# Optimization experiments

Hardware: AMD Instinct MI355X
Metric: run time of the kernel (lower is better)

The kernel has to match this reference:

```python
import jax, jax.numpy as jnp
import numpy as np

SHAPES = ((100, 100), (50, 50), (25, 25), (13, 13))
LENS = [h * w for h, w in SHAPES]
STARTS = [0]
for n in LENS[:-1]:
    STARTS.append(STARTS[-1] + n)
S_TOT = sum(LENS)  # 13294
B, C, HH, DH, L, P, NQ, NL, FF = 2, 256, 8, 32, 4, 4, 300, 6, 1024
WH = np.array([[w, h] for h, w in SHAPES], np.float32)  # [L,2] (W,H) offset normalizer


def ln(x, g, b):
    m = x.mean(-1, keepdims=True)
    v = ((x - m) ** 2).mean(-1, keepdims=True)
    return (x - m) * jax.lax.rsqrt(v + 1e-5) * g + b


def bilinear(v, grid):
    # v: [N,Hl,Wl,D]; grid: [N,Q,2] in [-1,1]; grid_sample bilinear, align_corners=False, zero padding
    N, Hl, Wl, Dd = v.shape
    x = (grid[..., 0] + 1.0) * 0.5 * Wl - 0.5
    y = (grid[..., 1] + 1.0) * 0.5 * Hl - 0.5
    x0f = jnp.floor(x); y0f = jnp.floor(y)
    wx = x - x0f; wy = y - y0f
    x0 = x0f.astype(jnp.int32); y0 = y0f.astype(jnp.int32)
    vf = v.reshape(N, Hl * Wl, Dd)
    def g(yi, xi):
        valid = (yi >= 0) & (yi < Hl) & (xi >= 0) & (xi < Wl)
        idx = jnp.clip(yi, 0, Hl - 1) * Wl + jnp.clip(xi, 0, Wl - 1)
        return jnp.take_along_axis(vf, idx[..., None], axis=1) * valid[..., None]
    return (((1 - wy) * (1 - wx))[..., None] * g(y0, x0)
            + ((1 - wy) * wx)[..., None] * g(y0, x0 + 1)
            + (wy * (1 - wx))[..., None] * g(y0 + 1, x0)
            + (wy * wx)[..., None] * g(y0 + 1, x0 + 1))


def msda(query, ref, src, so_w, so_b, aw_w, aw_b, vp_w, vp_b, op_w, op_b):
    # query:[B,Lq,C] ref:[B,Lq,L,2] src:[B,S,C]
    Bq, Lq, _ = query.shape
    value = (src @ vp_w.T + vp_b).reshape(Bq, S_TOT, HH, DH)
    offs = (query @ so_w.T + so_b).reshape(Bq, Lq, HH, L, P, 2)
    aw = jax.nn.softmax((query @ aw_w.T + aw_b).reshape(Bq, Lq, HH, L * P), -1)
    aw = aw.reshape(Bq, Lq, HH, L, P)
    loc = ref[:, :, None, :, None, :] + offs / jnp.asarray(WH)[None, None, None, :, None, :]
    grid = 2.0 * loc - 1.0  # [B,Lq,HH,L,P,2]
    out = jnp.zeros((Bq, HH, Lq, DH), query.dtype)
    for l, (Hl, Wl) in enumerate(SHAPES):
        st = STARTS[l]
        v_l = value[:, st:st + Hl * Wl].reshape(Bq, Hl, Wl, HH, DH).transpose(0, 3, 1, 2, 4).reshape(Bq * HH, Hl, Wl, DH)
        g_l = grid[:, :, :, l].transpose(0, 2, 1, 3, 4).reshape(Bq * HH, Lq * P, 2)
        s = bilinear(v_l, g_l).reshape(Bq, HH, Lq, P, DH)
        out = out + jnp.einsum('bqhp,bhqpd->bhqd', aw[:, :, :, l], s)
    out = out.transpose(0, 2, 1, 3).reshape(Bq, Lq, C)
    return out @ op_w.T + op_b


def enc_ref_points():
    refs = []
    for Hl, Wl in SHAPES:
        ry = (jnp.arange(Hl, dtype=jnp.float32) + 0.5) / Hl
        rx = (jnp.arange(Wl, dtype=jnp.float32) + 0.5) / Wl
        gy, gx = jnp.meshgrid(ry, rx, indexing='ij')
        refs.append(jnp.stack([gx.reshape(-1), gy.reshape(-1)], -1))
    r = jnp.concatenate(refs, 0)  # [S,2]; valid_ratios == 1 (no padding)
    return jnp.broadcast_to(r[None, :, None, :], (B, S_TOT, L, 2))


def _forward(src_flatten, pos_flatten, query_embed, level_embed, refp_w, refp_b,
             eso_w, eso_b, eaw_w, eaw_b, evp_w, evp_b, eop_w, eop_b,
             en1_g, en1_b, el1_w, el1_b, el2_w, el2_b, en2_g, en2_b,
             dso_w, dso_b, daw_w, daw_b, dvp_w, dvp_b, dop_w, dop_b,
             dsa_in_w, dsa_in_b, dsa_out_w, dsa_out_b,
             dn1_g, dn1_b, dn2_g, dn2_b, dn3_g, dn3_b,
             dl1_w, dl1_b, dl2_w, dl2_b):
    lev = jnp.concatenate([jnp.broadcast_to(level_embed[l], (LENS[l], C)) for l in range(L)], 0)
    pos = pos_flatten + lev[None]
    memory = src_flatten
    eref = enc_ref_points()
    for i in range(NL):  # encoder
        q = memory + pos
        m2 = msda(q, eref, memory, eso_w[i], eso_b[i], eaw_w[i], eaw_b[i], evp_w[i], evp_b[i], eop_w[i], eop_b[i])
        memory = ln(memory + m2, en1_g[i], en1_b[i])
        f = jax.nn.relu(memory @ el1_w[i].T + el1_b[i]) @ el2_w[i].T + el2_b[i]
        memory = ln(memory + f, en2_g[i], en2_b[i])
    qpos, tgt = jnp.split(query_embed, 2, axis=-1)
    qpos = jnp.broadcast_to(qpos[None], (B, NQ, C))
    tgt = jnp.broadcast_to(tgt[None], (B, NQ, C))
    ref = jax.nn.sigmoid(qpos @ refp_w.T + refp_b)  # [B,NQ,2]
    init_ref = ref
    ref_in = jnp.broadcast_to(ref[:, :, None, :], (B, NQ, L, 2))
    scale = 1.0 / np.sqrt(DH)
    for i in range(NL):  # decoder
        q = tgt + qpos
        wq, wk, wv = jnp.split(dsa_in_w[i], 3, 0)
        bq, bk, bv = jnp.split(dsa_in_b[i], 3, 0)
        qh = (q @ wq.T + bq).reshape(B, NQ, HH, DH).transpose(0, 2, 1, 3)
        kh = (q @ wk.T + bk).reshape(B, NQ, HH, DH).transpose(0, 2, 1, 3)
        vh = (tgt @ wv.T + bv).reshape(B, NQ, HH, DH).transpose(0, 2, 1, 3)
        att = jax.nn.softmax(jnp.einsum('bhqd,bhkd->bhqk', qh, kh) * scale, -1)
        sa = jnp.einsum('bhqk,bhkd->bhqd', att, vh).transpose(0, 2, 1, 3).reshape(B, NQ, C)
        sa = sa @ dsa_out_w[i].T + dsa_out_b[i]
        tgt = ln(tgt + sa, dn2_g[i], dn2_b[i])
        ca = msda(tgt + qpos, ref_in, memory, dso_w[i], dso_b[i], daw_w[i], daw_b[i], dvp_w[i], dvp_b[i], dop_w[i], dop_b[i])
        tgt = ln(tgt + ca, dn1_g[i], dn1_b[i])
        f = jax.nn.relu(tgt @ dl1_w[i].T + dl1_b[i]) @ dl2_w[i].T + dl2_b[i]
        tgt = ln(tgt + f, dn3_g[i], dn3_b[i])
    return tgt, init_ref, ref


def setup_inputs() -> dict:
    ks = iter(jax.random.split(jax.random.key(0), 80))
    def rn(shape, s=0.02):
        return jax.random.normal(next(ks), shape, jnp.float32) * s
    z = lambda shape: jnp.zeros(shape, jnp.float32)
    o = lambda shape: jnp.ones(shape, jnp.float32)
    HLP2, HLP = HH * L * P * 2, HH * L * P
    return {
        'src_flatten': rn((B, S_TOT, C), 1.0),
        'pos_flatten': rn((B, S_TOT, C), 1.0),
        'query_embed': rn((NQ, 2 * C), 1.0),
        'level_embed': rn((L, C), 1.0),
        'refp_w': rn((2, C)), 'refp_b': z((2,)),
        'eso_w': rn((NL, HLP2, C)), 'eso_b': z((NL, HLP2)),
        'eaw_w': rn((NL, HLP, C)), 'eaw_b': z((NL, HLP)),
        'evp_w': rn((NL, C, C)), 'evp_b': z((NL, C)),
        'eop_w': rn((NL, C, C)), 'eop_b': z((NL, C)),
        'en1_g': o((NL, C)), 'en1_b': z((NL, C)),
        'el1_w': rn((NL, FF, C)), 'el1_b': z((NL, FF)),
        'el2_w': rn((NL, C, FF)), 'el2_b': z((NL, C)),
        'en2_g': o((NL, C)), 'en2_b': z((NL, C)),
        'dso_w': rn((NL, HLP2, C)), 'dso_b': z((NL, HLP2)),
        'daw_w': rn((NL, HLP, C)), 'daw_b': z((NL, HLP)),
        'dvp_w': rn((NL, C, C)), 'dvp_b': z((NL, C)),
        'dop_w': rn((NL, C, C)), 'dop_b': z((NL, C)),
        'dsa_in_w': rn((NL, 3 * C, C)), 'dsa_in_b': z((NL, 3 * C)),
        'dsa_out_w': rn((NL, C, C)), 'dsa_out_b': z((NL, C)),
        'dn1_g': o((NL, C)), 'dn1_b': z((NL, C)),
        'dn2_g': o((NL, C)), 'dn2_b': z((NL, C)),
        'dn3_g': o((NL, C)), 'dn3_b': z((NL, C)),
        'dl1_w': rn((NL, FF, C)), 'dl1_b': z((NL, FF)),
        'dl2_w': rn((NL, C, FF)), 'dl2_b': z((NL, C)),
    }


def reference(src_flatten, pos_flatten, query_embed, level_embed, refp_w, refp_b,
              eso_w, eso_b, eaw_w, eaw_b, evp_w, evp_b, eop_w, eop_b,
              en1_g, en1_b, el1_w, el1_b, el2_w, el2_b, en2_g, en2_b,
              dso_w, dso_b, daw_w, daw_b, dvp_w, dvp_b, dop_w, dop_b,
              dsa_in_w, dsa_in_b, dsa_out_w, dsa_out_b,
              dn1_g, dn1_b, dn2_g, dn2_b, dn3_g, dn3_b,
              dl1_w, dl1_b, dl2_w, dl2_b):
    return _forward(src_flatten, pos_flatten, query_embed, level_embed, refp_w, refp_b,
                    eso_w, eso_b, eaw_w, eaw_b, evp_w, evp_b, eop_w, eop_b,
                    en1_g, en1_b, el1_w, el1_b, el2_w, el2_b, en2_g, en2_b,
                    dso_w, dso_b, daw_w, daw_b, dvp_w, dvp_b, dop_w, dop_b,
                    dsa_in_w, dsa_in_b, dsa_out_w, dsa_out_b,
                    dn1_g, dn1_b, dn2_g, dn2_b, dn3_g, dn3_b,
                    dl1_w, dl1_b, dl2_w, dl2_b)
```

## Files before the change

kernel.cpp:

```cpp
#include <hip/hip_runtime.h>

static constexpr int kS  = 13294;
static constexpr int kB  = 2;
static constexpr int kBS = kB * kS;
static constexpr int kC  = 256;
static constexpr int kH  = 8;
static constexpr int kNQ = 300;
static constexpr int kFF = 1024;
static constexpr int kNL = 6;

using short8 = __attribute__((ext_vector_type(8))) short;
using f32x4  = __attribute__((ext_vector_type(4))) float;

__device__ __forceinline__ unsigned short f2b(float f) {
  unsigned u = __builtin_bit_cast(unsigned, f);
  return (unsigned short)((u + 0x7FFF + ((u >> 16) & 1)) >> 16);
}
__device__ __forceinline__ float bf2f(unsigned short u) {
  return __builtin_bit_cast(float, ((unsigned)u) << 16);
}
__device__ __forceinline__ float bflo(unsigned u) {
  return __builtin_bit_cast(float, u << 16);
}
__device__ __forceinline__ float bfhi(unsigned u) {
  return __builtin_bit_cast(float, u & 0xFFFF0000u);
}

#if defined(__has_builtin)
#if __has_builtin(__builtin_amdgcn_global_load_lds)
#define HAS_GLL 1
#endif
#endif
#ifndef HAS_GLL
#define HAS_GLL 0
#endif

#if HAS_GLL
typedef const __attribute__((address_space(1))) void* gas_t;
typedef __attribute__((address_space(3))) void* las_t;
#define GLOAD16(gp, lp) __builtin_amdgcn_global_load_lds((gas_t)(gp), (las_t)(lp), 16, 0, 0)
#endif


template<int ACT, int OBF>
__global__ __launch_bounds__(256) void gemm_mfma(
    const unsigned short* __restrict__ A, const unsigned short* __restrict__ Wt,
    const float* __restrict__ bias, void* __restrict__ outp, int M, int N, int K) {
  __shared__ __align__(16) unsigned short As[128 * 64];
  __shared__ __align__(16) unsigned short Bs[128 * 64];
  const int t = threadIdx.x;
  const int nB = N >> 7;
  const int tot = gridDim.x;
  const int q8 = tot >> 3, r8 = tot & 7;
  const int xcd = blockIdx.x & 7, pos = blockIdx.x >> 3;
  const int wg = (xcd < r8 ? xcd * (q8 + 1) : r8 * (q8 + 1) + (xcd - r8) * q8) + pos;
  const int m0 = (wg / nB) * 128, n0 = (wg % nB) * 128;
  const int wid = t >> 6, lane = t & 63;
  const int wr = wid >> 1, wc = wid & 1;
  const int srow = t >> 3;
  const int scol = (((t & 7) ^ (srow & 7)) * 8);
  const int lr = lane & 15;
  const int q4 = lane >> 4;
  const int e7 = lr & 7;

  f32x4 acc[4][4];
#pragma unroll
  for (int i = 0; i < 4; ++i)
#pragma unroll
    for (int j = 0; j < 4; ++j) acc[i][j] = (f32x4){0.f, 0.f, 0.f, 0.f};

  for (int k0 = 0; k0 < K; k0 += 64) {
#if HAS_GLL
    __syncthreads();
#pragma unroll
    for (int c = 0; c < 4; ++c) {
      int ar = m0 + c * 32 + srow; if (ar >= M) ar = M - 1;
      GLOAD16(A + (size_t)ar * K + k0 + scol, (char*)As + c * 4096 + t * 16);
      int br = n0 + c * 32 + srow; if (br >= N) br = N - 1;
      GLOAD16(Wt + (size_t)br * K + k0 + scol, (char*)Bs + c * 4096 + t * 16);
    }
    __syncthreads();
#else
    short8 ta[4], tb[4];
#pragma unroll
    for (int c = 0; c < 4; ++c) {
      int ar = m0 + c * 32 + srow; if (ar >= M) ar = M - 1;
      ta[c] = *(const short8*)(A + (size_t)ar * K + k0 + scol);
      int br = n0 + c * 32 + srow; if (br >= N) br = N - 1;
      tb[c] = *(const short8*)(Wt + (size_t)br * K + k0 + scol);
    }
    __syncthreads();
#pragma unroll
    for (int c = 0; c < 4; ++c) {
      *(short8*)&As[c * 2048 + t * 8] = ta[c];
      *(short8*)&Bs[c * 2048 + t * 8] = tb[c];
    }
    __syncthreads();
#endif
#pragma unroll
    for (int kk = 0; kk < 2; ++kk) {
      const int pg = (((kk << 2) + q4) ^ e7) * 8;
      short8 af[4], bf[4];
#pragma unroll
      for (int mi = 0; mi < 4; ++mi)
        af[mi] = *(const short8*)&As[(wr * 64 + mi * 16 + lr) * 64 + pg];
#pragma unroll
      for (int ni = 0; ni < 4; ++ni)
        bf[ni] = *(const short8*)&Bs[(wc * 64 + ni * 16 + lr) * 64 + pg];
#pragma unroll
      for (int mi = 0; mi < 4; ++mi)
#pragma unroll
        for (int ni = 0; ni < 4; ++ni)
          acc[mi][ni] = __builtin_amdgcn_mfma_f32_16x16x32_bf16(af[mi], bf[ni], acc[mi][ni], 0, 0, 0);
    }
  }
  const int orow0 = m0 + wr * 64;
  const int ocol = n0 + wc * 64 + lr;
  float bv[4];
#pragma unroll
  for (int ni = 0; ni < 4; ++ni) bv[ni] = bias[ocol + ni * 16];
#pragma unroll
  for (int mi = 0; mi < 4; ++mi) {
#pragma unroll
    for (int j = 0; j < 4; ++j) {
      const int r = orow0 + mi * 16 + q4 * 4 + j;
      if (r < M) {
#pragma unroll
        for (int ni = 0; ni < 4; ++ni) {
          float v = acc[mi][ni][j] + bv[ni];
          if (ACT) v = fmaxf(v, 0.f);
          if (OBF) ((unsigned short*)outp)[(size_t)r * N + ocol + ni * 16] = f2b(v);
          else     ((float*)outp)[(size_t)r * N + ocol + ni * 16] = v;
        }
      }
    }
  }
}

template<int ACT, int OBF>
__global__ __launch_bounds__(256) void gemm_mfma_s(
    const unsigned short* __restrict__ A, const unsigned short* __restrict__ Wt,
    const float* __restrict__ bias, void* __restrict__ outp, int M, int N, int K) {
  __shared__ __align__(16) unsigned short As[64 * 64];
  __shared__ __align__(16) unsigned short Bs[64 * 64];
  const int t = threadIdx.x;
  const int m0 = blockIdx.y * 64, n0 = blockIdx.x * 64;
  const int wid = t >> 6, lane = t & 63;
  const int wr = wid >> 1, wc = wid & 1;
  const int srow = t >> 3;
  const int scol = (((t & 7) ^ (srow & 7)) * 8);
  const int lr = lane & 15;
  const int q4 = lane >> 4;
  const int e7 = lr & 7;

  f32x4 acc[2][2];
#pragma unroll
  for (int i = 0; i < 2; ++i)
#pragma unroll
    for (int j = 0; j < 2; ++j) acc[i][j] = (f32x4){0.f, 0.f, 0.f, 0.f};

  for (int k0 = 0; k0 < K; k0 += 64) {
#if HAS_GLL
    __syncthreads();
#pragma unroll
    for (int c = 0; c < 2; ++c) {
      int ar = m0 + c * 32 + srow; if (ar >= M) ar = M - 1;
      GLOAD16(A + (size_t)ar * K + k0 + scol, (char*)As + c * 4096 + t * 16);
      int br = n0 + c * 32 + srow; if (br >= N) br = N - 1;
      GLOAD16(Wt + (size_t)br * K + k0 + scol, (char*)Bs + c * 4096 + t * 16);
    }
    __syncthreads();
#else
    short8 ta[2], tb[2];
#pragma unroll
    for (int c = 0; c < 2; ++c) {
      int ar = m0 + c * 32 + srow; if (ar >= M) ar = M - 1;
      ta[c] = *(const short8*)(A + (size_t)ar * K + k0 + scol);
      int br = n0 + c * 32 + srow; if (br >= N) br = N - 1;
      tb[c] = *(const short8*)(Wt + (size_t)br * K + k0 + scol);
    }
    __syncthreads();
#pragma unroll
    for (int c = 0; c < 2; ++c) {
      *(short8*)&As[c * 2048 + t * 8] = ta[c];
      *(short8*)&Bs[c * 2048 + t * 8] = tb[c];
    }
    __syncthreads();
#endif
#pragma unroll
    for (int kk = 0; kk < 2; ++kk) {
      const int pg = (((kk << 2) + q4) ^ e7) * 8;
      short8 af[2], bf[2];
#pragma unroll
      for (int mi = 0; mi < 2; ++mi)
        af[mi] = *(const short8*)&As[(wr * 32 + mi * 16 + lr) * 64 + pg];
#pragma unroll
      for (int ni = 0; ni < 2; ++ni)
        bf[ni] = *(const short8*)&Bs[(wc * 32 + ni * 16 + lr) * 64 + pg];
#pragma unroll
      for (int mi = 0; mi < 2; ++mi)
#pragma unroll
        for (int ni = 0; ni < 2; ++ni)
          acc[mi][ni] = __builtin_amdgcn_mfma_f32_16x16x32_bf16(af[mi], bf[ni], acc[mi][ni], 0, 0, 0);
    }
  }
  const int orow0 = m0 + wr * 32;
  const int ocol = n0 + wc * 32 + lr;
  float bv[2];
#pragma unroll
  for (int ni = 0; ni < 2; ++ni) bv[ni] = bias[ocol + ni * 16];
#pragma unroll
  for (int mi = 0; mi < 2; ++mi) {
#pragma unroll
    for (int j = 0; j < 4; ++j) {
      const int r = orow0 + mi * 16 + q4 * 4 + j;
      if (r < M) {
#pragma unroll
        for (int ni = 0; ni < 2; ++ni) {
          float v = acc[mi][ni][j] + bv[ni];
          if (ACT) v = fmaxf(v, 0.f);
          if (OBF) ((unsigned short*)outp)[(size_t)r * N + ocol + ni * 16] = f2b(v);
          else     ((float*)outp)[(size_t)r * N + ocol + ni * 16] = v;
        }
      }
    }
  }
}

template<int WRITEQ, int WRITEF>
__global__ __launch_bounds__(256) void gemm_ln_k(
    const unsigned short* __restrict__ A, const unsigned short* __restrict__ Wt,
    const float* __restrict__ bias, const unsigned short* __restrict__ x_bf,
    const float* __restrict__ g, const float* __restrict__ be,
    float* __restrict__ outf, unsigned short* __restrict__ outb,
    unsigned short* __restrict__ qout, const unsigned short* __restrict__ poslev,
    int M, int K) {
  __shared__ __align__(16) unsigned short As[32 * 64];
  __shared__ __align__(16) unsigned short Bs[256 * 64];
  __shared__ float rsum[32][4], rsq[32][4], rmv[32][2];
  const int t = threadIdx.x;
  const int m0 = blockIdx.x * 32;
  const int wid = t >> 6, lane = t & 63;
  const int srow = t >> 3;
  const int scol = (((t & 7) ^ (srow & 7)) * 8);
  const int lr = lane & 15;
  const int q4 = lane >> 4;
  const int e7 = lr & 7;

  f32x4 acc[2][4];
#pragma unroll
  for (int i = 0; i < 2; ++i)
#pragma unroll
    for (int j = 0; j < 4; ++j) acc[i][j] = (f32x4){0.f, 0.f, 0.f, 0.f};

  for (int k0 = 0; k0 < K; k0 += 64) {
#if HAS_GLL
    __syncthreads();
    {
      int ar = m0 + srow; if (ar >= M) ar = M - 1;
      GLOAD16(A + (size_t)ar * K + k0 + scol, (char*)As + t * 16);
    }
#pragma unroll
    for (int c = 0; c < 8; ++c) {
      GLOAD16(Wt + (size_t)(c * 32 + srow) * K + k0 + scol, (char*)Bs + c * 4096 + t * 16);
    }
    __syncthreads();
#else
    short8 ta, tb[8];
    {
      int ar = m0 + srow; if (ar >= M) ar = M - 1;
      ta = *(const short8*)(A + (size_t)ar * K + k0 + scol);
    }
#pragma unroll
    for (int c = 0; c < 8; ++c)
      tb[c] = *(const short8*)(Wt + (size_t)(c * 32 + srow) * K + k0 + scol);
    __syncthreads();
    *(short8*)&As[t * 8] = ta;
#pragma unroll
    for (int c = 0; c < 8; ++c) *(short8*)&Bs[c * 2048 + t * 8] = tb[c];
    __syncthreads();
#endif
#pragma unroll
    for (int kk = 0; kk < 2; ++kk) {
      const int pg = (((kk << 2) + q4) ^ e7) * 8;
      short8 af[2], bf[4];
#pragma unroll
      for (int mi = 0; mi < 2; ++mi)
        af[mi] = *(const short8*)&As[(mi * 16 + lr) * 64 + pg];
#pragma unroll
      for (int ni = 0; ni < 4; ++ni)
        bf[ni] = *(const short8*)&Bs[(wid * 64 + ni * 16 + lr) * 64 + pg];
#pragma unroll
      for (int mi = 0; mi < 2; ++mi)
#pragma unroll
        for (int ni = 0; ni < 4; ++ni)
          acc[mi][ni] = __builtin_amdgcn_mfma_f32_16x16x32_bf16(af[mi], bf[ni], acc[mi][ni], 0, 0, 0);
    }
  }
  float bv[4], gv[4], bev[4];
  int cols[4];
#pragma unroll
  for (int ni = 0; ni < 4; ++ni) {
    cols[ni] = wid * 64 + ni * 16 + lr;
    bv[ni] = bias[cols[ni]];
    gv[ni] = g[cols[ni]];
    bev[ni] = be[cols[ni]];
  }
#pragma unroll
  for (int mi = 0; mi < 2; ++mi) {
#pragma unroll
    for (int j = 0; j < 4; ++j) {
      const int brow = mi * 16 + q4 * 4 + j;
      int grow = m0 + brow; if (grow >= M) grow = M - 1;
      const unsigned short* xr = x_bf + (size_t)grow * 256;
      float s = 0.f, s2 = 0.f;
#pragma unroll
      for (int ni = 0; ni < 4; ++ni) {
        float v = acc[mi][ni][j] + bv[ni] + bf2f(xr[cols[ni]]);
        acc[mi][ni][j] = v;
        s += v; s2 += v * v;
      }
#pragma unroll
      for (int o = 1; o < 16; o <<= 1) {
        s += __shfl_xor(s, o);
        s2 += __shfl_xor(s2, o);
      }
      if (lr == 0) { rsum[brow][wid] = s; rsq[brow][wid] = s2; }
    }
  }
  __syncthreads();
  if (t < 32) {
    float s = rsum[t][0] + rsum[t][1] + rsum[t][2] + rsum[t][3];
    float s2 = rsq[t][0] + rsq[t][1] + rsq[t][2] + rsq[t][3];
    float mean = s * (1.f / 256.f);
    float var = s2 * (1.f / 256.f) - mean * mean;
    rmv[t][0] = mean;
    rmv[t][1] = rsqrtf(var + 1e-5f);
  }
  __syncthreads();
#pragma unroll
  for (int mi = 0; mi < 2; ++mi) {
#pragma unroll
    for (int j = 0; j < 4; ++j) {
      const int brow = mi * 16 + q4 * 4 + j;
      const int grow = m0 + brow;
      if (grow >= M) continue;
      const float mean = rmv[brow][0], rs = rmv[brow][1];
#pragma unroll
      for (int ni = 0; ni < 4; ++ni) {
        const float v = (acc[mi][ni][j] - mean) * rs * gv[ni] + bev[ni];
        const size_t oi = (size_t)grow * 256 + cols[ni];
        if (WRITEF) outf[oi] = v;
        outb[oi] = f2b(v);
        if (WRITEQ) qout[oi] = f2b(v + bf2f(poslev[oi]));
      }
    }
  }
}

__global__ void cast_bf_k(const float* __restrict__ in, unsigned short* __restrict__ out, int n4) {
  int i = blockIdx.x * 256 + threadIdx.x;
  if (i >= n4) return;
  float4 v = ((const float4*)in)[i];
  ushort4 o; o.x = f2b(v.x); o.y = f2b(v.y); o.z = f2b(v.z); o.w = f2b(v.w);
  ((ushort4*)out)[i] = o;
}

__global__ void pack_bias_k(const float* __restrict__ so_b, const float* __restrict__ aw_b,
                            float* __restrict__ fb) {
  int i = blockIdx.x * 256 + threadIdx.x;
  if (i >= kNL * 384) return;
  int l = i / 384, j = i - l * 384;
  fb[i] = (j < 256) ? so_b[l * 256 + j] : aw_b[l * 128 + j - 256];
}

__global__ void poslev_k(const float* __restrict__ pos, const float* __restrict__ lev,
                         unsigned short* __restrict__ out, int n4) {
  int i = blockIdx.x * 256 + threadIdx.x;
  if (i >= n4) return;
  int c4 = i & 63;
  int row = i >> 6;
  int s = row % kS;
  int l = (s < 10000) ? 0 : (s < 12500) ? 1 : (s < 13125) ? 2 : 3;
  float4 p = ((const float4*)pos)[i];
  float4 lv = ((const float4*)(lev + l * kC))[c4];
  ushort4 o;
  o.x = f2b(p.x + lv.x); o.y = f2b(p.y + lv.y);
  o.z = f2b(p.z + lv.z); o.w = f2b(p.w + lv.w);
  ((ushort4*)out)[i] = o;
}

__global__ void enc_q_k(const float* __restrict__ src, const unsigned short* __restrict__ poslev,
                        unsigned short* __restrict__ q, int n4) {
  int i = blockIdx.x * 256 + threadIdx.x;
  if (i >= n4) return;
  float4 m = ((const float4*)src)[i];
  ushort4 pl = ((const ushort4*)poslev)[i];
  ushort4 o;
  o.x = f2b(m.x + bf2f(pl.x)); o.y = f2b(m.y + bf2f(pl.y));
  o.z = f2b(m.z + bf2f(pl.z)); o.w = f2b(m.w + bf2f(pl.w));
  ((ushort4*)q)[i] = o;
}

__global__ void refs_k(float* __restrict__ refS) {
  int s = blockIdx.x * 256 + threadIdx.x;
  if (s >= kS) return;
  int st, W;
  if (s < 10000)      { st = 0;     W = 100; }
  else if (s < 12500) { st = 10000; W = 50; }
  else if (s < 13125) { st = 12500; W = 25; }
  else                { st = 13125; W = 13; }
  int idx = s - st;
  int y = idx / W;
  int x = idx - y * W;
  refS[s * 2 + 0] = (x + 0.5f) / (float)W;
  refS[s * 2 + 1] = (y + 0.5f) / (float)W;
}

__global__ __launch_bounds__(256) void msda_fused_k(
    const unsigned short* __restrict__ value, int vstride, int vcol,
    const unsigned short* __restrict__ foab, const float* __restrict__ refs,
    unsigned short* __restrict__ out, int Mq) {
  __shared__ int   sidx[16][2][kH][4];
  __shared__ float sw[16][2][kH][4];
  const int t = threadIdx.x;
  const int bq0 = blockIdx.x * 2;
  const int qq = t >> 7;
  {
    const int bq = bq0 + qq;
    const int b = (bq >= Mq) ? 1 : 0;
    const int qi = bq - b * Mq;
    const int h = (t >> 4) & 7, lp = t & 15, l = lp >> 2;
    const unsigned short* row = foab + (size_t)bq * 384;
    float logit = bf2f(row[256 + h * 16 + lp]);
    float mx = logit;
#pragma unroll
    for (int o = 1; o < 16; o <<= 1) mx = fmaxf(mx, __shfl_xor(mx, o));
    float e = __expf(logit - mx), ssum = e;
#pragma unroll
    for (int o = 1; o < 16; o <<= 1) ssum += __shfl_xor(ssum, o);
    const float a = e / ssum;
    const unsigned opair = *(const unsigned*)(row + h * 32 + lp * 2);
    const float offx = bflo(opair);
    const float offy = bfhi(opair);
    const float rx = refs[qi * 2 + 0];
    const float ry = refs[qi * 2 + 1];
    const int wtab[4] = {100, 50, 25, 13};
    const int stab[4] = {0, 10000, 12500, 13125};
    const int W = wtab[l];
    const int start = stab[l];
    const float px = fmaf(rx, (float)W, offx) - 0.5f;
    const float py = fmaf(ry, (float)W, offy) - 0.5f;
    const float fx = floorf(px), fy = floorf(py);
    const float wx = px - fx, wy = py - fy;
    const int x0 = (int)fx, y0 = (int)fy;
    const int x0c = min(max(x0, 0), W - 1);
    const int x1c = min(max(x0 + 1, 0), W - 1);
    const int y0c = min(max(y0, 0), W - 1);
    const int y1c = min(max(y0 + 1, 0), W - 1);
    const float vx0 = (x0 >= 0 && x0 < W) ? 1.f : 0.f;
    const float vx1 = (x0 + 1 >= 0 && x0 + 1 < W) ? 1.f : 0.f;
    const float vy0 = (y0 >= 0 && y0 < W) ? 1.f : 0.f;
    const float vy1 = (y0 + 1 >= 0 && y0 + 1 < W) ? 1.f : 0.f;
    const int base0 = b * kS * vstride + vcol + start * vstride;
    sidx[lp][qq][h][0] = base0 + (y0c * W + x0c) * vstride;
    sidx[lp][qq][h][1] = base0 + (y0c * W + x1c) * vstride;
    sidx[lp][qq][h][2] = base0 + (y1c * W + x0c) * vstride;
    sidx[lp][qq][h][3] = base0 + (y1c * W + x1c) * vstride;
    const float omwx = 1.f - wx, omwy = 1.f - wy;
    sw[lp][qq][h][0] = a * omwy * omwx * vy0 * vx0;
    sw[lp][qq][h][1] = a * omwy * wx * vy0 * vx1;
    sw[lp][qq][h][2] = a * wy * omwx * vy1 * vx0;
    sw[lp][qq][h][3] = a * wy * wx * vy1 * vx1;
  }
  __syncthreads();
  const int h = (t >> 4) & 7, dp = t & 15;
  const int bq = bq0 + qq;
  const int chan = h * 64 + dp * 4;
  const char* valc = (const char*)value;
  float aLo0 = 0.f, aLo1 = 0.f, aHi0 = 0.f, aHi1 = 0.f;
#pragma unroll
  for (int p0 = 0; p0 < 16; p0 += 8) {
    unsigned u[32];
    float w[32];
#pragma unroll
    for (int pp = 0; pp < 8; ++pp) {
      const int4 I = *(const int4*)&sidx[p0 + pp][qq][h][0];
      const float4 Wv = *(const float4*)&sw[p0 + pp][qq][h][0];
      u[pp * 4 + 0] = *(const unsigned*)(valc + (unsigned)(I.x + chan));
      u[pp * 4 + 1] = *(const unsigned*)(valc + (unsigned)(I.y + chan));
      u[pp * 4 + 2] = *(const unsigned*)(valc + (unsigned)(I.z + chan));
      u[pp * 4 + 3] = *(const unsigned*)(valc + (unsigned)(I.w + chan));
      w[pp * 4 + 0] = Wv.x; w[pp * 4 + 1] = Wv.y;
      w[pp * 4 + 2] = Wv.z; w[pp * 4 + 3] = Wv.w;
    }
#pragma unroll
    for (int j = 0; j < 32; j += 2) {
      aLo0 = fmaf(w[j], bflo(u[j]), aLo0);
      aHi0 = fmaf(w[j], bfhi(u[j]), aHi0);
      aLo1 = fmaf(w[j + 1], bflo(u[j + 1]), aLo1);
      aHi1 = fmaf(w[j + 1], bfhi(u[j + 1]), aHi1);
    }
  }
  const float accLo = aLo0 + aLo1;
  const float accHi = aHi0 + aHi1;
  const unsigned packed = (unsigned)f2b(accLo) | ((unsigned)f2b(accHi) << 16);
  ((unsigned*)out)[(size_t)bq * 128 + h * 16 + dp] = packed;
}

__global__ void add_bcast_bf_k(const float* __restrict__ a, const float* __restrict__ b,
                               unsigned short* __restrict__ out, int n4, int nb4) {
  int i = blockIdx.x * 256 + threadIdx.x;
  if (i >= n4) return;
  const float4 av = ((const float4*)a)[i];
  const float4 bv = ((const float4*)b)[i % nb4];
  ushort4 o;
  o.x = f2b(av.x + bv.x); o.y = f2b(av.y + bv.y);
  o.z = f2b(av.z + bv.z); o.w = f2b(av.w + bv.w);
  ((ushort4*)out)[i] = o;
}

__global__ void dec_init_k(const float* __restrict__ qe, float* __restrict__ tgt,
                           unsigned short* __restrict__ tgt_bf, float* __restrict__ qposb) {
  int i = blockIdx.x * 256 + threadIdx.x;
  if (i >= kNQ * kC) return;
  int q = i >> 8, c = i & 255;
  qposb[i] = qe[q * 512 + c];
  float tg = qe[q * 512 + 256 + c];
  tgt[i] = tg;
  tgt[kNQ * kC + i] = tg;
  unsigned short tb = f2b(tg);
  tgt_bf[i] = tb;
  tgt_bf[kNQ * kC + i] = tb;
}

__global__ __launch_bounds__(64) void ref_k(const float* __restrict__ qposb,
                                            const float* __restrict__ rw,
                                            const float* __restrict__ rb,
                                            float* __restrict__ ref300) {
  const int q = blockIdx.x;
  const int lane = threadIdx.x;
  const float4 qv = ((const float4*)(qposb + q * 256))[lane];
  const float4 w0 = ((const float4*)rw)[lane];
  const float4 w1 = ((const float4*)(rw + 256))[lane];
  float a0 = qv.x * w0.x + qv.y * w0.y + qv.z * w0.z + qv.w * w0.w;
  float a1 = qv.x * w1.x + qv.y * w1.y + qv.z * w1.z + qv.w * w1.w;
#pragma unroll
  for (int off = 32; off; off >>= 1) {
    a0 += __shfl_xor(a0, off);
    a1 += __shfl_xor(a1, off);
  }
  if (lane == 0) {
    ref300[q * 2 + 0] = 1.f / (1.f + __expf(-(a0 + rb[0])));
    ref300[q * 2 + 1] = 1.f / (1.f + __expf(-(a1 + rb[1])));
  }
}

__global__ __launch_bounds__(64) void dec_attn_k(const float* __restrict__ qk,
                                                 const float* __restrict__ v,
                                                 unsigned short* __restrict__ outp) {
  const int bid = blockIdx.x;
  const int q = bid % kNQ;
  const int bh = bid / kNQ;
  const int h = bh & 7;
  const int b = bh >> 3;
  const int lane = threadIdx.x;
  __shared__ float p[304];
  const float* qv = qk + ((size_t)(b * kNQ + q)) * 512 + h * 32;
  float qreg[32];
#pragma unroll
  for (int m = 0; m < 32; ++m) qreg[m] = qv[m];
  float scores[5];
  float mx = -1e30f;
#pragma unroll
  for (int j = 0; j < 5; ++j) {
    const int k = lane + j * 64;
    float sc = -1e30f;
    if (k < kNQ) {
      const float* kv = qk + ((size_t)(b * kNQ + k)) * 512 + 256 + h * 32;
      float acc = 0.f;
#pragma unroll
      for (int m = 0; m < 32; ++m) acc = fmaf(qreg[m], kv[m], acc);
      sc = acc * 0.17677669529663687f;
    }
    scores[j] = sc;
    mx = fmaxf(mx, sc);
  }
#pragma unroll
  for (int off = 32; off; off >>= 1) mx = fmaxf(mx, __shfl_xor(mx, off));
  float sum = 0.f;
#pragma unroll
  for (int j = 0; j < 5; ++j) {
    const int k = lane + j * 64;
    float e = 0.f;
    if (k < kNQ) e = __expf(scores[j] - mx);
    scores[j] = e;
    sum += e;
  }
#pragma unroll
  for (int off = 32; off; off >>= 1) sum += __shfl_xor(sum, off);
  const float inv = 1.f / sum;
#pragma unroll
  for (int j = 0; j < 5; ++j) {
    const int k = lane + j * 64;
    if (k < kNQ) p[k] = scores[j] * inv;
  }
  __syncthreads();
  const int d = lane & 31, half = lane >> 5;
  float acc = 0.f;
  for (int k = half * 150; k < half * 150 + 150; ++k)
    acc = fmaf(p[k], v[((size_t)(b * kNQ + k)) * 256 + h * 32 + d], acc);
  acc += __shfl_down(acc, 32);
  if (lane < 32) outp[((size_t)(b * kNQ + q)) * 256 + h * 32 + d] = f2b(acc);
}

__global__ void write_refs_k(const float* __restrict__ ref300, float* __restrict__ outp) {
  int i = blockIdx.x * 256 + threadIdx.x;
  if (i >= 1200) return;
  float v = ref300[i % 600];
  outp[153600 + i] = v;
  outp[154800 + i] = v;
}

__global__ void sentinel_k(float* __restrict__ outp) {
  if (threadIdx.x < 64) outp[threadIdx.x] = 12345.0f;
}

extern "C" void kernel_launch(void* const* d_in, const int* in_sizes, int n_in,
                              void* d_out, int out_size, void* d_ws, size_t ws_size,
                              hipStream_t stream) {
  const float* src      = (const float*)d_in[0];
  const float* pos      = (const float*)d_in[1];
  const float* qe       = (const float*)d_in[2];
  const float* lev      = (const float*)d_in[3];
  const float* refp_w   = (const float*)d_in[4];
  const float* refp_b   = (const float*)d_in[5];
  const float* eso_w    = (const float*)d_in[6];
  const float* eso_b    = (const float*)d_in[7];
  const float* eaw_w    = (const float*)d_in[8];
  const float* eaw_b    = (const float*)d_in[9];
  const float* evp_w    = (const float*)d_in[10];
  const float* evp_b    = (const float*)d_in[11];
  const float* eop_w    = (const float*)d_in[12];
  const float* eop_b    = (const float*)d_in[13];
  const float* en1_g    = (const float*)d_in[14];
  const float* en1_b    = (const float*)d_in[15];
  const float* el1_w    = (const float*)d_in[16];
  const float* el1_b    = (const float*)d_in[17];
  const float* el2_w    = (const float*)d_in[18];
  const float* el2_b    = (const float*)d_in[19];
  const float* en2_g    = (const float*)d_in[20];
  const float* en2_b    = (const float*)d_in[21];
  const float* dso_w    = (const float*)d_in[22];
  const float* dso_b    = (const float*)d_in[23];
  const float* daw_w    = (const float*)d_in[24];
  const float* daw_b    = (const float*)d_in[25];
  const float* dvp_w    = (const float*)d_in[26];
  const float* dvp_b    = (const float*)d_in[27];
  const float* dop_w    = (const float*)d_in[28];
  const float* dop_b    = (const float*)d_in[29];
  const float* dsa_in_w = (const float*)d_in[30];
  const float* dsa_in_b = (const float*)d_in[31];
  const float* dsa_out_w= (const float*)d_in[32];
  const float* dsa_out_b= (const float*)d_in[33];
  const float* dn1_g    = (const float*)d_in[34];
  const float* dn1_b    = (const float*)d_in[35];
  const float* dn2_g    = (const float*)d_in[36];
  const float* dn2_b    = (const float*)d_in[37];
  const float* dn3_g    = (const float*)d_in[38];
  const float* dn3_b    = (const float*)d_in[39];
  const float* dl1_w    = (const float*)d_in[40];
  const float* dl1_b    = (const float*)d_in[41];
  const float* dl2_w    = (const float*)d_in[42];
  const float* dl2_b    = (const float*)d_in[43];

  float* Wsp = (float*)d_ws;
  size_t off = 0;
  auto alloc = [&](size_t n) { float* p = Wsp + off; off += n; return p; };
  const size_t NBC = (size_t)kBS * kC;
  unsigned short* memory_bf = (unsigned short*)alloc(NBC / 2);
  unsigned short* poslev_bf = (unsigned short*)alloc(NBC / 2);
  float* r2       = alloc(NBC);
  unsigned short* val_bf = (unsigned short*)r2;
  float* r3       = alloc(NBC / 2);
  unsigned short* qbuf_bf = (unsigned short*)r3;
  unsigned short* sampbuf_bf = (unsigned short*)r3;
  float* r4       = alloc(NBC * 2);
  unsigned short* foab_bf = (unsigned short*)r4;
  unsigned short* hid_bf = (unsigned short*)r4;
  unsigned short* val_all = (unsigned short*)r2;
  float* refS     = alloc((size_t)kS * 2 + 2);
  auto allocb = [&](size_t elems) { return (unsigned short*)alloc(elems / 2); };
  unsigned short* fesoawW = allocb((size_t)kNL * 384 * 256);
  unsigned short* evpW  = allocb((size_t)kNL * 65536);
  unsigned short* eopW  = allocb((size_t)kNL * 65536);
  unsigned short* el1W  = allocb((size_t)kNL * 262144);
  unsigned short* el2W  = allocb((size_t)kNL * 262144);
  unsigned short* fdsoawW = allocb((size_t)kNL * 384 * 256);
  unsigned short* dvpW  = allocb((size_t)kNL * 65536);
  unsigned short* dopW  = allocb((size_t)kNL * 65536);
  unsigned short* dsaiW = allocb((size_t)kNL * 196608);
  unsigned short* dsaoW = allocb((size_t)kNL * 65536);
  unsigned short* dl1W  = allocb((size_t)kNL * 262144);
  unsigned short* dl2W  = allocb((size_t)kNL * 262144);
  float* fbias_e  = alloc((size_t)kNL * 384);
  float* fbias_d  = alloc((size_t)kNL * 384);
  const size_t NQC = (size_t)kB * kNQ * kC;
  float* tgt      = alloc(NQC);
  unsigned short* tgt_bf = (unsigned short*)alloc(NQC / 2);
  float* qposb    = alloc((size_t)kNQ * kC);
  unsigned short* dq_bf = (unsigned short*)alloc(NQC / 2);
  float* qkbuf    = alloc(NQC * 2);
  float* vbuf     = alloc(NQC);
  unsigned short* sabuf_bf = (unsigned short*)alloc(NQC / 2);
  unsigned short* dfoab_bf = (unsigned short*)alloc((size_t)kB * kNQ * 384 / 2);
  unsigned short* dsamp_bf = (unsigned short*)alloc(NQC / 2);
  unsigned short* dffnh_bf = (unsigned short*)alloc((size_t)kB * kNQ * kFF / 2);
  float* ref300   = alloc(600);

  if (ws_size < off * sizeof(float)) {
    hipLaunchKernelGGL(sentinel_k, dim3(1), dim3(64), 0, stream, (float*)d_out);
    return;
  }

  auto GEMM = [&](const unsigned short* A, const unsigned short* Wt, const float* bias,
                  void* out, int M, int N, int K, int variant) {
    dim3 g((N / 128) * ((M + 127) / 128));
    if (variant == 1)
      hipLaunchKernelGGL((gemm_mfma<1, 1>), g, dim3(256), 0, stream, A, Wt, bias, out, M, N, K);
    else if (variant == 2)
      hipLaunchKernelGGL((gemm_mfma<0, 1>), g, dim3(256), 0, stream, A, Wt, bias, out, M, N, K);
    else
      hipLaunchKernelGGL((gemm_mfma<0, 0>), g, dim3(256), 0, stream, A, Wt, bias, out, M, N, K);
  };
  auto GEMMS = [&](const unsigned short* A, const unsigned short* Wt, const float* bias,
                   void* out, int M, int N, int K, int variant) {
    dim3 g(N / 64, (M + 63) / 64);
    if (variant == 1)
      hipLaunchKernelGGL((gemm_mfma_s<1, 1>), g, dim3(256), 0, stream, A, Wt, bias, out, M, N, K);
    else if (variant == 2)
      hipLaunchKernelGGL((gemm_mfma_s<0, 1>), g, dim3(256), 0, stream, A, Wt, bias, out, M, N, K);
    else
      hipLaunchKernelGGL((gemm_mfma_s<0, 0>), g, dim3(256), 0, stream, A, Wt, bias, out, M, N, K);
  };
  auto CASTW = [&](const float* srcw, unsigned short* dstw, size_t elems) {
    int n4 = (int)(elems / 4);
    hipLaunchKernelGGL(cast_bf_k, dim3((n4 + 255) / 256), dim3(256), 0, stream, srcw, dstw, n4);
  };

  for (int i = 0; i < kNL; ++i) {
    CASTW(eso_w + (size_t)i * 65536, fesoawW + (size_t)i * 98304, 65536);
    CASTW(eaw_w + (size_t)i * 32768, fesoawW + (size_t)i * 98304 + 65536, 32768);
    CASTW(dso_w + (size_t)i * 65536, fdsoawW + (size_t)i * 98304, 65536);
    CASTW(daw_w + (size_t)i * 32768, fdsoawW + (size_t)i * 98304 + 65536, 32768);
  }
  CASTW(evp_w, evpW, (size_t)kNL * 65536);
  CASTW(eop_w, eopW, (size_t)kNL * 65536);
  CASTW(el1_w, el1W, (size_t)kNL * 262144);
  CASTW(el2_w, el2W, (size_t)kNL * 262144);
  CASTW(dvp_w, dvpW, (size_t)kNL * 65536);
  CASTW(dop_w, dopW, (size_t)kNL * 65536);
  CASTW(dsa_in_w, dsaiW, (size_t)kNL * 196608);
  CASTW(dsa_out_w, dsaoW, (size_t)kNL * 65536);
  CASTW(dl1_w, dl1W, (size_t)kNL * 262144);
  CASTW(dl2_w, dl2W, (size_t)kNL * 262144);
  hipLaunchKernelGGL(pack_bias_k, dim3((kNL * 384 + 255) / 256), dim3(256), 0, stream,
                     eso_b, eaw_b, fbias_e);
  hipLaunchKernelGGL(pack_bias_k, dim3((kNL * 384 + 255) / 256), dim3(256), 0, stream,
                     dso_b, daw_b, fbias_d);
  const int n4full = kBS * 64;
  hipLaunchKernelGGL(cast_bf_k, dim3((n4full + 255) / 256), dim3(256), 0, stream,
                     src, memory_bf, n4full);
  hipLaunchKernelGGL(poslev_k, dim3((n4full + 255) / 256), dim3(256), 0, stream,
                     pos, lev, poslev_bf, n4full);
  hipLaunchKernelGGL(refs_k, dim3((kS + 255) / 256), dim3(256), 0, stream, refS);
  hipLaunchKernelGGL(enc_q_k, dim3((n4full + 255) / 256), dim3(256), 0, stream,
                     src, poslev_bf, qbuf_bf, n4full);

  const int grid_ln = (kBS + 31) / 32;
  for (int i = 0; i < kNL; ++i) {
    GEMM(memory_bf, evpW + (size_t)i * 65536, evp_b + i * kC, val_bf, kBS, 256, 256, 2);
    GEMM(qbuf_bf, fesoawW + (size_t)i * 98304, fbias_e + i * 384, foab_bf, kBS, 384, 256, 2);
    hipLaunchKernelGGL(msda_fused_k, dim3(kBS / 2), dim3(256), 0, stream,
                       val_bf, 512, 0, foab_bf, refS, sampbuf_bf, kS);
    hipLaunchKernelGGL((gemm_ln_k<0, 0>), dim3(grid_ln), dim3(256), 0, stream,
                       sampbuf_bf, eopW + (size_t)i * 65536, eop_b + i * kC,
                       memory_bf, en1_g + i * kC, en1_b + i * kC,
                       (float*)nullptr, memory_bf, (unsigned short*)nullptr,
                       (const unsigned short*)nullptr, kBS, 256);
    GEMM(memory_bf, el1W + (size_t)i * 262144, el1_b + i * kFF, hid_bf, kBS, 1024, 256, 1);
    hipLaunchKernelGGL((gemm_ln_k<1, 0>), dim3(grid_ln), dim3(256), 0, stream,
                       hid_bf, el2W + (size_t)i * 262144, el2_b + i * kC,
                       memory_bf, en2_g + i * kC, en2_b + i * kC,
                       (float*)nullptr, memory_bf, qbuf_bf, poslev_bf, kBS, 1024);
  }

  hipLaunchKernelGGL(dec_init_k, dim3(300), dim3(256), 0, stream, qe, tgt, tgt_bf, qposb);
  hipLaunchKernelGGL(ref_k, dim3(kNQ), dim3(64), 0, stream, qposb, refp_w, refp_b, ref300);
  GEMM(memory_bf, dvpW, dvp_b, val_all, kBS, kNL * 256, 256, 2);

  const int dn4 = kB * kNQ * 64;
  const int qn4 = kNQ * 64;
  const int MD = kB * kNQ;
  const int grid_lnd = (MD + 31) / 32;
  for (int i = 0; i < kNL; ++i) {
    hipLaunchKernelGGL(add_bcast_bf_k, dim3((dn4 + 255) / 256), dim3(256), 0, stream,
                       tgt, qposb, dq_bf, dn4, qn4);
    GEMMS(dq_bf, dsaiW + (size_t)i * 196608, dsa_in_b + i * 768, qkbuf, MD, 512, 256, 0);
    GEMMS(tgt_bf, dsaiW + (size_t)i * 196608 + (size_t)512 * 256,
          dsa_in_b + i * 768 + 512, vbuf, MD, 256, 256, 0);
    hipLaunchKernelGGL(dec_attn_k, dim3(kB * kH * kNQ), dim3(64), 0, stream,
                       qkbuf, vbuf, sabuf_bf);
    hipLaunchKernelGGL((gemm_ln_k<0, 1>), dim3(grid_lnd), dim3(256), 0, stream,
                       sabuf_bf, dsaoW + (size_t)i * 65536, dsa_out_b + i * kC,
                       tgt_bf, dn2_g + i * kC, dn2_b + i * kC,
                       tgt, tgt_bf, (unsigned short*)nullptr,
                       (const unsigned short*)nullptr, MD, 256);
    hipLaunchKernelGGL(add_bcast_bf_k, dim3((dn4 + 255) / 256), dim3(256), 0, stream,
                       tgt, qposb, dq_bf, dn4, qn4);
    GEMMS(dq_bf, fdsoawW + (size_t)i * 98304, fbias_d + i * 384, dfoab_bf, MD, 384, 256, 2);
    hipLaunchKernelGGL(msda_fused_k, dim3(MD / 2), dim3(256), 0, stream,
                       val_all, kNL * 512, i * 512, dfoab_bf, ref300, dsamp_bf, kNQ);
    hipLaunchKernelGGL((gemm_ln_k<0, 1>), dim3(grid_lnd), dim3(256), 0, stream,
                       dsamp_bf, dopW + (size_t)i * 65536, dop_b + i * kC,
                       tgt_bf, dn1_g + i * kC, dn1_b + i * kC,
                       tgt, tgt_bf, (unsigned short*)nullptr,
                       (const unsigned short*)nullptr, MD, 256);
    GEMMS(tgt_bf, dl1W + (size_t)i * 262144, dl1_b + i * kFF, dffnh_bf, MD, 1024, 256, 1);
    hipLaunchKernelGGL((gemm_ln_k<0, 1>), dim3(grid_lnd), dim3(256), 0, stream,
                       dffnh_bf, dl2W + (size_t)i * 262144, dl2_b + i * kC,
                       tgt_bf, dn3_g + i * kC, dn3_b + i * kC,
                       tgt, tgt_bf, (unsigned short*)nullptr,
                       (const unsigned short*)nullptr, MD, 1024);
  }

  hipMemcpyAsync(d_out, tgt, NQC * sizeof(float), hipMemcpyDeviceToDevice, stream);
  hipLaunchKernelGGL(write_refs_k, dim3(5), dim3(256), 0, stream, ref300, (float*)d_out);
}
```

Before: 1.794 ms.

## Load GEMM-LN operands directly from global memory into MFMA fragments

Removes the shared-memory staging of A and weight tiles in the fused GEMM+LayerNorm kernel. Each lane now loads its MFMA fragments straight from global memory, stepping K by 32 with an unroll of 4. This drops the per-tile barriers and LDS traffic. In exchange, each A row is fetched redundantly by all four warps and loads become less coalesced, relying on the cache hierarchy to absorb the extra traffic.

```diff
diff --git a/kernel.cpp b/kernel.cpp
--- a/kernel.cpp
+++ b/kernel.cpp
@@ -235,17 +235,23 @@
     float* __restrict__ outf, unsigned short* __restrict__ outb,
     unsigned short* __restrict__ qout, const unsigned short* __restrict__ poslev,
     int M, int K) {
-  __shared__ __align__(16) unsigned short As[32 * 64];
-  __shared__ __align__(16) unsigned short Bs[256 * 64];
   __shared__ float rsum[32][4], rsq[32][4], rmv[32][2];
   const int t = threadIdx.x;
   const int m0 = blockIdx.x * 32;
   const int wid = t >> 6, lane = t & 63;
-  const int srow = t >> 3;
-  const int scol = (((t & 7) ^ (srow & 7)) * 8);
   const int lr = lane & 15;
   const int q4 = lane >> 4;
-  const int e7 = lr & 7;
+
+  const unsigned short* aptr[2];
+#pragma unroll
+  for (int mi = 0; mi < 2; ++mi) {
+    int ar = m0 + mi * 16 + lr; if (ar >= M) ar = M - 1;
+    aptr[mi] = A + (size_t)ar * K;
+  }
+  const unsigned short* bptr[4];
+#pragma unroll
+  for (int ni = 0; ni < 4; ++ni)
+    bptr[ni] = Wt + (size_t)(wid * 64 + ni * 16 + lr) * K;
 
   f32x4 acc[2][4];
 #pragma unroll
@@ -253,50 +259,21 @@
 #pragma unroll
     for (int j = 0; j < 4; ++j) acc[i][j] = (f32x4){0.f, 0.f, 0.f, 0.f};
 
-  for (int k0 = 0; k0 < K; k0 += 64) {
-#if HAS_GLL
-    __syncthreads();
-    {
-      int ar = m0 + srow; if (ar >= M) ar = M - 1;
-      GLOAD16(A + (size_t)ar * K + k0 + scol, (char*)As + t * 16);
-    }
-#pragma unroll
-    for (int c = 0; c < 8; ++c) {
-      GLOAD16(Wt + (size_t)(c * 32 + srow) * K + k0 + scol, (char*)Bs + c * 4096 + t * 16);
-    }
-    __syncthreads();
-#else
-    short8 ta, tb[8];
-    {
-      int ar = m0 + srow; if (ar >= M) ar = M - 1;
-      ta = *(const short8*)(A + (size_t)ar * K + k0 + scol);
-    }
-#pragma unroll
-    for (int c = 0; c < 8; ++c)
-      tb[c] = *(const short8*)(Wt + (size_t)(c * 32 + srow) * K + k0 + scol);
-    __syncthreads();
-    *(short8*)&As[t * 8] = ta;
-#pragma unroll
-    for (int c = 0; c < 8; ++c) *(short8*)&Bs[c * 2048 + t * 8] = tb[c];
-    __syncthreads();
-#endif
-#pragma unroll
-    for (int kk = 0; kk < 2; ++kk) {
-      const int pg = (((kk << 2) + q4) ^ e7) * 8;
-      short8 af[2], bf[4];
-#pragma unroll
-      for (int mi = 0; mi < 2; ++mi)
-        af[mi] = *(const short8*)&As[(mi * 16 + lr) * 64 + pg];
+#pragma unroll 4
+  for (int k0 = 0; k0 < K; k0 += 32) {
+    const int ko = k0 + q4 * 8;
+    short8 af[2], bf[4];
+#pragma unroll
+    for (int mi = 0; mi < 2; ++mi) af[mi] = *(const short8*)(aptr[mi] + ko);
+#pragma unroll
+    for (int ni = 0; ni < 4; ++ni) bf[ni] = *(const short8*)(bptr[ni] + ko);
+#pragma unroll
+    for (int mi = 0; mi < 2; ++mi)
 #pragma unroll
       for (int ni = 0; ni < 4; ++ni)
-        bf[ni] = *(const short8*)&Bs[(wid * 64 + ni * 16 + lr) * 64 + pg];
-#pragma unroll
-      for (int mi = 0; mi < 2; ++mi)
-#pragma unroll
-        for (int ni = 0; ni < 4; ++ni)
-          acc[mi][ni] = __builtin_amdgcn_mfma_f32_16x16x32_bf16(af[mi], bf[ni], acc[mi][ni], 0, 0, 0);
-    }
-  }
+        acc[mi][ni] = __builtin_amdgcn_mfma_f32_16x16x32_bf16(af[mi], bf[ni], acc[mi][ni], 0, 0, 0);
+  }
+
   float bv[4], gv[4], bev[4];
   int cols[4];
 #pragma unroll
```

New measurement: 2.180 ms. +21.5%, slower.
